# Kernel tuning notes

Hardware: AMD Instinct MI355X
Metric: run time of the kernel (lower is better)

Reference implementation:

```python
import jax, jax.numpy as jnp
import numpy as np

B, S, HID = 1, 2048, 2048
H, KH, D = 16, 8, 128          # query heads, kv heads, head_dim
GROUPS = H // KH                # num_key_value_groups = 2
EPS = 1e-6
SCALE = D ** -0.5
NEG = -1e9


def rmsnorm(x, w):
    # torch.nn.RMSNorm over last dim with learned weight
    return x * jax.lax.rsqrt(jnp.mean(x * x, axis=-1, keepdims=True) + EPS) * w


def rope(x, cos, sin):
    # x: [b, s, h, d]; cos/sin: [s, d//2]  (rotate-half style, matching apply_rotary_emb_single)
    half = x.shape[-1] // 2
    xr, xi = x[..., :half], x[..., half:]
    c = cos[None, :, None, :]
    s = sin[None, :, None, :]
    return jnp.concatenate([xr * c - xi * s, xr * s + xi * c], axis=-1)


def setup_inputs() -> dict:
    key = jax.random.key(0)
    ks = jax.random.split(key, 8)
    hidden_states = jax.random.normal(ks[0], (B, S, HID), jnp.float32)
    # real RoPE angle tables (theta=1e6, Qwen3-style), shape [S, D//2]
    inv_freq = 1.0 / (1e6 ** (np.arange(0, D, 2, dtype=np.float32) / D))
    ang = np.arange(S, dtype=np.float32)[:, None] * inv_freq[None, :]
    freqs_cos = jnp.asarray(np.cos(ang), jnp.float32)
    freqs_sin = jnp.asarray(np.sin(ang), jnp.float32)
    # additive causal mask [1, S, S]
    causal = jnp.tril(jnp.ones((S, S), jnp.bool_))
    atten_mask = jnp.where(causal, 0.0, NEG).astype(jnp.float32)[None]
    # learned params (no bias: attention_bias=False)
    Wq = jax.random.normal(ks[1], (H * D, HID), jnp.float32) * 0.02
    Wk = jax.random.normal(ks[2], (KH * D, HID), jnp.float32) * 0.02
    Wv = jax.random.normal(ks[3], (KH * D, HID), jnp.float32) * 0.02
    Wo = jax.random.normal(ks[4], (HID, H * D), jnp.float32) * 0.02
    q_norm_w = 1.0 + 0.01 * jax.random.normal(ks[5], (D,), jnp.float32)
    k_norm_w = 1.0 + 0.01 * jax.random.normal(ks[6], (D,), jnp.float32)
    return {"hidden_states": hidden_states, "freqs_cos": freqs_cos, "freqs_sin": freqs_sin,
            "atten_mask": atten_mask, "Wq": Wq, "Wk": Wk, "Wv": Wv, "Wo": Wo,
            "q_norm_w": q_norm_w, "k_norm_w": k_norm_w}


def reference(hidden_states, freqs_cos, freqs_sin, atten_mask, Wq, Wk, Wv, Wo, q_norm_w, k_norm_w):
    b, s, _ = hidden_states.shape
    q = (hidden_states @ Wq.T).reshape(b, s, H, D)
    k = (hidden_states @ Wk.T).reshape(b, s, KH, D)
    v = (hidden_states @ Wv.T).reshape(b, s, KH, D)
    q = rope(rmsnorm(q, q_norm_w), freqs_cos, freqs_sin)
    k = rope(rmsnorm(k, k_norm_w), freqs_cos, freqs_sin)
    # GQA: head i uses kv head i // GROUPS -> repeat kv heads in-order
    k_exp = jnp.repeat(k, GROUPS, axis=2)  # [b, s, H, d]
    v_exp = jnp.repeat(v, GROUPS, axis=2)
    scores = jnp.einsum('bshd,bthd->bhst', q, k_exp) * SCALE + atten_mask[:, None, :, :]
    attn = jax.nn.softmax(scores, axis=-1)
    y = jnp.einsum('bhst,bthd->bshd', attn, v_exp).reshape(b, s, H * D)
    y = y @ Wo.T
    # output_new_cache_only: last-position k (post-norm/RoPE) and raw v per kv head
    k_new = jnp.transpose(k[:, -1], (1, 0, 2))  # [KH, b, D]
    v_new = jnp.transpose(v[:, -1], (1, 0, 2))  # [KH, b, D]
    return y, k_new, v_new
```

## Files before the change

### kernel.cpp

```cpp
#include <hip/hip_runtime.h>
#include <hip/hip_bf16.h>
#include <math.h>

#define S_LEN 2048
#define HID 2048
#define NH 16
#define NKH 8
#define HD 128
#define QKV_N 4096
#define SCALE 0.08838834764831845f
#define EPS 1e-6f
#define LOG2E 1.4426950408889634f

typedef __hip_bfloat16 bf16;
typedef unsigned int u32;
typedef __bf16 bf16x8 __attribute__((ext_vector_type(8)));
typedef float f32x4 __attribute__((ext_vector_type(4)));

#define MFMA(a, b, c) __builtin_amdgcn_mfma_f32_16x16x32_bf16(a, b, c, 0, 0, 0)

static __device__ __forceinline__ bf16x8 ld_frag(const bf16* p) {
    return __builtin_bit_cast(bf16x8, *(const uint4*)p);
}

static __device__ __forceinline__ void gload_lds16(const void* g, void* l) {
    __builtin_amdgcn_global_load_lds(
        (const __attribute__((address_space(1))) u32*)g,
        (__attribute__((address_space(3))) u32*)l, 16, 0, 0);
}

__global__ __launch_bounds__(256) void cvt4(
    const float* __restrict__ s0, const float* __restrict__ s1,
    const float* __restrict__ s2, const float* __restrict__ s3,
    bf16* __restrict__ d0, bf16* __restrict__ d1,
    bf16* __restrict__ d2, bf16* __restrict__ d3)
{
    int i = blockIdx.x * 256 + threadIdx.x;
    const float* s; bf16* d; int off;
    if (i < (1 << 20))                   { s = s0; d = d0; off = 0; }
    else if (i < (2 << 20))              { s = s1; d = d1; off = 1 << 20; }
    else if (i < (2 << 20) + (1 << 19))  { s = s2; d = d2; off = 2 << 20; }
    else                                 { s = s3; d = d3; off = (2 << 20) + (1 << 19); }
    int j = i - off;
    float4 v = ((const float4*)s)[j];
    bf16* p = d + 4 * (size_t)j;
    p[0] = __float2bfloat16(v.x);
    p[1] = __float2bfloat16(v.y);
    p[2] = __float2bfloat16(v.z);
    p[3] = __float2bfloat16(v.w);
}

__global__ __launch_bounds__(256) void cvt_bf16(
    const float* __restrict__ src, bf16* __restrict__ dst, int n4)
{
    int i = blockIdx.x * 256 + threadIdx.x;
    if (i < n4) {
        float4 v = ((const float4*)src)[i];
        bf16* d = dst + 4 * (size_t)i;
        d[0] = __float2bfloat16(v.x);
        d[1] = __float2bfloat16(v.y);
        d[2] = __float2bfloat16(v.z);
        d[3] = __float2bfloat16(v.w);
    }
}

template <int BF16OUT>
__global__ __launch_bounds__(256) void gemm_m97(
    const bf16* __restrict__ A, const bf16* __restrict__ B,
    void* __restrict__ Cv, int M, int N, int K)
{
    __shared__ bf16 As[128 * 32];
    __shared__ bf16 Bs[128 * 32];
    const int tid = threadIdx.x;
    const int n0 = blockIdx.x * 128, m0 = blockIdx.y * 128;
    const int w = tid >> 6, lane = tid & 63;
    const int l15 = lane & 15, quad = lane >> 4;
    const int wr = (w >> 1) * 64, wc = (w & 1) * 64;

    f32x4 acc[4][4];
    #pragma unroll
    for (int i = 0; i < 4; ++i)
        #pragma unroll
        for (int j = 0; j < 4; ++j)
            acc[i][j] = f32x4{0.f, 0.f, 0.f, 0.f};

    const int grow = lane >> 2;
    const int gcol = ((lane & 3) ^ ((lane >> 3) & 3)) * 8;
    const int fcol = (quad ^ ((l15 >> 1) & 3)) * 8;

    for (int k0 = 0; k0 < K; k0 += 32) {
        __syncthreads();
        #pragma unroll
        for (int j = 0; j < 2; ++j) {
            int c = 2 * w + j;
            int row = 16 * c + grow;
            gload_lds16(A + (size_t)(m0 + row) * K + k0 + gcol, &As[c * 512]);
            gload_lds16(B + (size_t)(n0 + row) * K + k0 + gcol, &Bs[c * 512]);
        }
        __syncthreads();

        bf16x8 av[4], bv[4];
        #pragma unroll
        for (int i = 0; i < 4; ++i)
            av[i] = ld_frag(&As[(wr + i * 16 + l15) * 32 + fcol]);
        #pragma unroll
        for (int j = 0; j < 4; ++j)
            bv[j] = ld_frag(&Bs[(wc + j * 16 + l15) * 32 + fcol]);
        #pragma unroll
        for (int i = 0; i < 4; ++i)
            #pragma unroll
            for (int j = 0; j < 4; ++j)
                acc[i][j] = MFMA(av[i], bv[j], acc[i][j]);
    }

    #pragma unroll
    for (int i = 0; i < 4; ++i)
        #pragma unroll
        for (int j = 0; j < 4; ++j)
            #pragma unroll
            for (int r = 0; r < 4; ++r) {
                int row = m0 + wr + i * 16 + quad * 4 + r;
                int col = n0 + wc + j * 16 + l15;
                if (BF16OUT)
                    ((bf16*)Cv)[(size_t)row * N + col] = __float2bfloat16(acc[i][j][r]);
                else
                    ((float*)Cv)[(size_t)row * N + col] = acc[i][j][r];
            }
}

__global__ __launch_bounds__(256, 3) void gemm_n64(
    const bf16* __restrict__ A, const bf16* __restrict__ B,
    float* __restrict__ C, int M, int N, int K)
{
    __shared__ bf16 As[128 * 32];
    __shared__ bf16 Bs[64 * 32];
    const int tid = threadIdx.x;
    const int n0 = blockIdx.x * 64, m0 = blockIdx.y * 128;
    const int w = tid >> 6, lane = tid & 63;
    const int l15 = lane & 15, quad = lane >> 4;

    f32x4 acc[2][4];
    #pragma unroll
    for (int i = 0; i < 2; ++i)
        #pragma unroll
        for (int j = 0; j < 4; ++j)
            acc[i][j] = f32x4{0.f, 0.f, 0.f, 0.f};

    const int grow = lane >> 2;
    const int gcol = ((lane & 3) ^ ((lane >> 3) & 3)) * 8;
    const int fcol = (quad ^ ((l15 >> 1) & 3)) * 8;

    for (int k0 = 0; k0 < K; k0 += 32) {
        __syncthreads();
        #pragma unroll
        for (int j = 0; j < 3; ++j) {
            int c = 3 * w + j;
            if (c < 8) {
                int row = 16 * c + grow;
                gload_lds16(A + (size_t)(m0 + row) * K + k0 + gcol, &As[c * 512]);
            } else {
                int row = 16 * (c - 8) + grow;
                gload_lds16(B + (size_t)(n0 + row) * K + k0 + gcol, &Bs[(c - 8) * 512]);
            }
        }
        __syncthreads();

        bf16x8 av[2], bv[4];
        #pragma unroll
        for (int i = 0; i < 2; ++i)
            av[i] = ld_frag(&As[(w * 32 + i * 16 + l15) * 32 + fcol]);
        #pragma unroll
        for (int j = 0; j < 4; ++j)
            bv[j] = ld_frag(&Bs[(j * 16 + l15) * 32 + fcol]);
        #pragma unroll
        for (int i = 0; i < 2; ++i)
            #pragma unroll
            for (int j = 0; j < 4; ++j)
                acc[i][j] = MFMA(av[i], bv[j], acc[i][j]);
    }

    #pragma unroll
    for (int i = 0; i < 2; ++i)
        #pragma unroll
        for (int j = 0; j < 4; ++j)
            #pragma unroll
            for (int r = 0; r < 4; ++r)
                C[(size_t)(m0 + w * 32 + i * 16 + quad * 4 + r) * N +
                  n0 + j * 16 + l15] = acc[i][j][r];
}

__global__ __launch_bounds__(128) void norm_rope(
    bf16* __restrict__ qkvb,
    const float* __restrict__ cosb, const float* __restrict__ sinb,
    const float* __restrict__ qw, const float* __restrict__ kw,
    float* __restrict__ knew, float* __restrict__ vnew)
{
    const int s = blockIdx.x;
    const int h = blockIdx.y;
    const int d = threadIdx.x;

    bf16* row;
    const float* wgt;
    int kh = -1;
    if (h < NH) {
        row = qkvb + (size_t)s * QKV_N + h * HD;
        wgt = qw;
    } else {
        kh = h - NH;
        row = qkvb + (size_t)s * QKV_N + HID + kh * HD;
        wgt = kw;
    }

    float x = __bfloat162float(row[d]);
    float ss = x * x;
    #pragma unroll
    for (int off = 32; off >= 1; off >>= 1) ss += __shfl_xor(ss, off, 64);

    __shared__ float sred[2];
    __shared__ float xn[128];
    int lane = d & 63, wid = d >> 6;
    if (lane == 0) sred[wid] = ss;
    __syncthreads();
    float total = sred[0] + sred[1];
    float rr = rsqrtf(total * (1.0f / 128.0f) + EPS);
    xn[d] = x * rr * wgt[d];
    __syncthreads();

    float res;
    if (d < 64) {
        float c = cosb[s * 64 + d], sn = sinb[s * 64 + d];
        res = xn[d] * c - xn[d + 64] * sn;
    } else {
        int d2 = d - 64;
        float c = cosb[s * 64 + d2], sn = sinb[s * 64 + d2];
        res = xn[d2] * sn + xn[d] * c;
    }

    float store_val = (h < NH) ? res * SCALE : res;
    row[d] = __float2bfloat16(store_val);

    if (kh >= 0 && s == S_LEN - 1) {
        knew[kh * HD + d] = res;
        vnew[kh * HD + d] =
            __bfloat162float(qkvb[(size_t)s * QKV_N + HID + NKH * HD + kh * HD + d]);
    }
}

__global__ __launch_bounds__(256) void transpose_v(
    const bf16* __restrict__ qkvb, bf16* __restrict__ vT)
{
    const int r0 = blockIdx.x * 64;
    const int s0 = blockIdx.y * 32;
    const int rl = threadIdx.x & 63, sg = threadIdx.x >> 6;

    union { uint4 u; bf16 b[8]; } pk;
    #pragma unroll
    for (int j = 0; j < 8; ++j)
        pk.b[j] = qkvb[(size_t)(s0 + sg * 8 + j) * QKV_N + HID + NKH * HD + r0 + rl];
    *(uint4*)(vT + (size_t)(r0 + rl) * S_LEN + s0 + sg * 8) = pk.u;
}

__global__ __launch_bounds__(256, 2) void attn_mfma(
    const bf16* __restrict__ qkvb, const bf16* __restrict__ vT,
    bf16* __restrict__ outb)
{
    __shared__ bf16 Ks[2][64 * 128];
    __shared__ bf16 Vs[2][128 * 64];
    __shared__ bf16 Ps[4][16 * 72];

    const int x = blockIdx.x;
    const int h = blockIdx.y, kvh = h >> 1;
    int a = (x & 1) ? (31 - (x >> 1)) : (x >> 1);
    const int qb = (h < 8) ? a : 31 - a;
    const int tid = threadIdx.x, w = tid >> 6, lane = tid & 63;
    const int l15 = lane & 15, quad = lane >> 4;
    const int qw0 = qb * 64 + w * 16;

    bf16x8 qf[4];
    #pragma unroll
    for (int dk = 0; dk < 4; ++dk)
        qf[dk] = ld_frag(qkvb + (size_t)(qw0 + l15) * QKV_N +
                         h * HD + dk * 32 + quad * 8);

    f32x4 o[8];
    #pragma unroll
    for (int dt = 0; dt < 8; ++dt) o[dt] = f32x4{0.f, 0.f, 0.f, 0.f};
    float m_st = -1e30f, l_st = 0.f;

    auto stage = [&](int t, int nb) {
        const int kt0 = t * 64;
        if (w < 2) {
            #pragma unroll
            for (int c = 0; c < 8; ++c) {
                int chunk = w * 8 + c;
                int row = 4 * chunk + (lane >> 4);
                int ls = (lane & 15) ^ (row & 15);
                gload_lds16(qkvb + (size_t)(kt0 + row) * QKV_N + HID +
                            kvh * HD + ls * 8,
                            &Ks[nb][chunk * 512]);
            }
        } else {
            #pragma unroll
            for (int c = 0; c < 8; ++c) {
                int chunk = (w - 2) * 8 + c;
                int row = 8 * chunk + (lane >> 3);
                int ls = (lane & 7) ^ ((lane >> 3) & 7);
                gload_lds16(vT + (size_t)(kvh * HD + row) * S_LEN + kt0 + ls * 8,
                            &Vs[nb][chunk * 512]);
            }
        }
    };

    stage(0, 0);

    for (int t = 0; t <= qb; ++t) {
        const int pp = t & 1;
        __syncthreads();
        if (t < qb) stage(t + 1, pp ^ 1);

        f32x4 sc[4];
        #pragma unroll
        for (int mt = 0; mt < 4; ++mt) sc[mt] = f32x4{0.f, 0.f, 0.f, 0.f};
        #pragma unroll
        for (int dk = 0; dk < 4; ++dk)
            #pragma unroll
            for (int mt = 0; mt < 4; ++mt) {
                bf16x8 kf = ld_frag(&Ks[pp][(mt * 16 + l15) * 128 +
                                            (((dk * 4 + quad) ^ l15) * 8)]);
                sc[mt] = MFMA(kf, qf[dk], sc[mt]);
            }

        if (t == qb) {
            #pragma unroll
            for (int mt = 0; mt < 4; ++mt)
                #pragma unroll
                for (int r = 0; r < 4; ++r) {
                    int kg = t * 64 + mt * 16 + quad * 4 + r;
                    if (kg > qw0 + l15) sc[mt][r] = -1e30f;
                }
        }

        float mx = -1e30f;
        #pragma unroll
        for (int mt = 0; mt < 4; ++mt)
            #pragma unroll
            for (int r = 0; r < 4; ++r) mx = fmaxf(mx, sc[mt][r]);
        mx = fmaxf(mx, __shfl_xor(mx, 16, 64));
        mx = fmaxf(mx, __shfl_xor(mx, 32, 64));
        float mnew = fmaxf(m_st, mx);
        float al = exp2f((m_st - mnew) * LOG2E);
        m_st = mnew;
        float rs = 0.f;
        #pragma unroll
        for (int mt = 0; mt < 4; ++mt) {
            union { uint2 u; bf16 hh[4]; } pk;
            #pragma unroll
            for (int r = 0; r < 4; ++r) {
                float p = exp2f((sc[mt][r] - mnew) * LOG2E);
                pk.hh[r] = __float2bfloat16(p);
                rs += p;
            }
            *(uint2*)&Ps[w][l15 * 72 + mt * 16 + quad * 4] = pk.u;
        }
        rs += __shfl_xor(rs, 16, 64);
        rs += __shfl_xor(rs, 32, 64);
        l_st = l_st * al + rs;

        #pragma unroll
        for (int dt = 0; dt < 8; ++dt)
            #pragma unroll
            for (int r = 0; r < 4; ++r) o[dt][r] *= al;

        #pragma unroll
        for (int kc = 0; kc < 2; ++kc) {
            bf16x8 pf = ld_frag(&Ps[w][l15 * 72 + kc * 32 + quad * 8]);
            #pragma unroll
            for (int dt = 0; dt < 8; ++dt) {
                bf16x8 vf = ld_frag(&Vs[pp][(dt * 16 + l15) * 64 +
                                            (((kc * 4 + quad) ^ (l15 & 7)) * 8)]);
                o[dt] = MFMA(vf, pf, o[dt]);
            }
        }
    }

    float inv = 1.0f / l_st;
    int qg = qw0 + l15;
    #pragma unroll
    for (int dt = 0; dt < 8; ++dt) {
        union { uint2 u; bf16 hh[4]; } pk;
        #pragma unroll
        for (int r = 0; r < 4; ++r)
            pk.hh[r] = __float2bfloat16(o[dt][r] * inv);
        *(uint2*)&outb[(size_t)qg * HID + h * HD + dt * 16 + quad * 4] = pk.u;
    }
}

extern "C" void kernel_launch(void* const* d_in, const int* in_sizes, int n_in,
                              void* d_out, int out_size, void* d_ws, size_t ws_size,
                              hipStream_t stream) {
    const float* hidden = (const float*)d_in[0];
    const float* fcos   = (const float*)d_in[1];
    const float* fsin   = (const float*)d_in[2];
    const float* Wq = (const float*)d_in[4];
    const float* Wk = (const float*)d_in[5];
    const float* Wv = (const float*)d_in[6];
    const float* Wo = (const float*)d_in[7];
    const float* qw = (const float*)d_in[8];
    const float* kw = (const float*)d_in[9];
    float* out = (float*)d_out;

    bf16* qkvb  = (bf16*)d_ws;
    bf16* vT    = qkvb + (size_t)S_LEN * QKV_N;
    bf16* attnb = vT + (size_t)NKH * HD * S_LEN;
    bf16* wqkvb = attnb + (size_t)S_LEN * HID;
    bf16* hidb  = wqkvb + (size_t)QKV_N * HID;

    float* knew = out + (size_t)S_LEN * HID;
    float* vnew = knew + NKH * HD;

    cvt4<<<12288, 256, 0, stream>>>(
        hidden, Wq, Wk, Wv,
        hidb, wqkvb, wqkvb + (size_t)HID * HID,
        wqkvb + (size_t)(HID + NKH * HD) * HID);

    gemm_m97<1><<<dim3(QKV_N / 128, S_LEN / 128), 256, 0, stream>>>(
        hidb, wqkvb, qkvb, S_LEN, QKV_N, HID);

    cvt_bf16<<<(HID * HID / 4) / 256, 256, 0, stream>>>(Wo, hidb, HID * HID / 4);

    norm_rope<<<dim3(S_LEN, NH + NKH), 128, 0, stream>>>(
        qkvb, fcos, fsin, qw, kw, knew, vnew);

    transpose_v<<<dim3((NKH * HD) / 64, S_LEN / 32), 256, 0, stream>>>(qkvb, vT);

    attn_mfma<<<dim3(32, NH), 256, 0, stream>>>(qkvb, vT, attnb);

    gemm_n64<<<dim3(HID / 64, S_LEN / 128), 256, 0, stream>>>(
        attnb, hidb, out, S_LEN, HID, HID);
}
```

Measured before the change: 293.6 us.

## Fuse norm, RoPE and V transpose into QKV GEMM epilogue; shrink attention KV tile

The QKV GEMM now gives each warp full 128-column head rows, so RMSNorm, RoPE and scaling run in its epilogue. V tiles are written transposed directly, which removes the norm_rope and transpose_v kernels. The Wo conversion is folded into the single conversion kernel, using a separate buffer. Attention switches to 32-key tiles with smaller LDS, occupancy 3, and per-warp skipping of fully masked tiles. The GEMM warp layout changes from 2x2 to 4x1, which needs more B-fragment LDS reads, and the attention loop now runs twice as many iterations, each with a sync.

```diff
diff --git a/kernel.cpp b/kernel.cpp
--- a/kernel.cpp
+++ b/kernel.cpp
@@ -29,18 +29,20 @@
         (__attribute__((address_space(3))) u32*)l, 16, 0, 0);
 }
 
-__global__ __launch_bounds__(256) void cvt4(
+__global__ __launch_bounds__(256) void cvt5(
     const float* __restrict__ s0, const float* __restrict__ s1,
     const float* __restrict__ s2, const float* __restrict__ s3,
-    bf16* __restrict__ d0, bf16* __restrict__ d1,
-    bf16* __restrict__ d2, bf16* __restrict__ d3)
+    const float* __restrict__ s4,
+    bf16* __restrict__ d0, bf16* __restrict__ d1, bf16* __restrict__ d2,
+    bf16* __restrict__ d3, bf16* __restrict__ d4)
 {
     int i = blockIdx.x * 256 + threadIdx.x;
     const float* s; bf16* d; int off;
     if (i < (1 << 20))                   { s = s0; d = d0; off = 0; }
     else if (i < (2 << 20))              { s = s1; d = d1; off = 1 << 20; }
     else if (i < (2 << 20) + (1 << 19))  { s = s2; d = d2; off = 2 << 20; }
-    else                                 { s = s3; d = d3; off = (2 << 20) + (1 << 19); }
+    else if (i < (3 << 20))              { s = s3; d = d3; off = (2 << 20) + (1 << 19); }
+    else                                 { s = s4; d = d4; off = 3 << 20; }
     int j = i - off;
     float4 v = ((const float4*)s)[j];
     bf16* p = d + 4 * (size_t)j;
@@ -50,24 +52,12 @@
     p[3] = __float2bfloat16(v.w);
 }
 
-__global__ __launch_bounds__(256) void cvt_bf16(
-    const float* __restrict__ src, bf16* __restrict__ dst, int n4)
-{
-    int i = blockIdx.x * 256 + threadIdx.x;
-    if (i < n4) {
-        float4 v = ((const float4*)src)[i];
-        bf16* d = dst + 4 * (size_t)i;
-        d[0] = __float2bfloat16(v.x);
-        d[1] = __float2bfloat16(v.y);
-        d[2] = __float2bfloat16(v.z);
-        d[3] = __float2bfloat16(v.w);
-    }
-}
-
-template <int BF16OUT>
-__global__ __launch_bounds__(256) void gemm_m97(
+__global__ __launch_bounds__(256) void gemm_qkv(
     const bf16* __restrict__ A, const bf16* __restrict__ B,
-    void* __restrict__ Cv, int M, int N, int K)
+    bf16* __restrict__ qkvb, bf16* __restrict__ vT,
+    const float* __restrict__ fcos, const float* __restrict__ fsin,
+    const float* __restrict__ qw, const float* __restrict__ kw,
+    float* __restrict__ knew, float* __restrict__ vnew)
 {
     __shared__ bf16 As[128 * 32];
     __shared__ bf16 Bs[128 * 32];
@@ -75,57 +65,108 @@
     const int n0 = blockIdx.x * 128, m0 = blockIdx.y * 128;
     const int w = tid >> 6, lane = tid & 63;
     const int l15 = lane & 15, quad = lane >> 4;
-    const int wr = (w >> 1) * 64, wc = (w & 1) * 64;
-
-    f32x4 acc[4][4];
-    #pragma unroll
-    for (int i = 0; i < 4; ++i)
-        #pragma unroll
-        for (int j = 0; j < 4; ++j)
+
+    f32x4 acc[2][8];
+    #pragma unroll
+    for (int i = 0; i < 2; ++i)
+        #pragma unroll
+        for (int j = 0; j < 8; ++j)
             acc[i][j] = f32x4{0.f, 0.f, 0.f, 0.f};
 
     const int grow = lane >> 2;
     const int gcol = ((lane & 3) ^ ((lane >> 3) & 3)) * 8;
     const int fcol = (quad ^ ((l15 >> 1) & 3)) * 8;
 
-    for (int k0 = 0; k0 < K; k0 += 32) {
+    for (int k0 = 0; k0 < HID; k0 += 32) {
         __syncthreads();
         #pragma unroll
         for (int j = 0; j < 2; ++j) {
             int c = 2 * w + j;
             int row = 16 * c + grow;
-            gload_lds16(A + (size_t)(m0 + row) * K + k0 + gcol, &As[c * 512]);
-            gload_lds16(B + (size_t)(n0 + row) * K + k0 + gcol, &Bs[c * 512]);
+            gload_lds16(A + (size_t)(m0 + row) * HID + k0 + gcol, &As[c * 512]);
+            gload_lds16(B + (size_t)(n0 + row) * HID + k0 + gcol, &Bs[c * 512]);
         }
         __syncthreads();
 
-        bf16x8 av[4], bv[4];
-        #pragma unroll
-        for (int i = 0; i < 4; ++i)
-            av[i] = ld_frag(&As[(wr + i * 16 + l15) * 32 + fcol]);
-        #pragma unroll
-        for (int j = 0; j < 4; ++j)
-            bv[j] = ld_frag(&Bs[(wc + j * 16 + l15) * 32 + fcol]);
-        #pragma unroll
-        for (int i = 0; i < 4; ++i)
-            #pragma unroll
-            for (int j = 0; j < 4; ++j)
+        bf16x8 av[2], bv[8];
+        #pragma unroll
+        for (int i = 0; i < 2; ++i)
+            av[i] = ld_frag(&As[(w * 32 + i * 16 + l15) * 32 + fcol]);
+        #pragma unroll
+        for (int j = 0; j < 8; ++j)
+            bv[j] = ld_frag(&Bs[(j * 16 + l15) * 32 + fcol]);
+        #pragma unroll
+        for (int i = 0; i < 2; ++i)
+            #pragma unroll
+            for (int j = 0; j < 8; ++j)
                 acc[i][j] = MFMA(av[i], bv[j], acc[i][j]);
     }
 
-    #pragma unroll
-    for (int i = 0; i < 4; ++i)
-        #pragma unroll
-        for (int j = 0; j < 4; ++j)
+    const int hblk = n0 >> 7;
+    if (hblk < 24) {
+        const float* wgt = (hblk < 16) ? qw : kw;
+        float wv[8];
+        #pragma unroll
+        for (int j = 0; j < 8; ++j) wv[j] = wgt[j * 16 + l15];
+        const size_t cb = (hblk < 16) ? (size_t)hblk * HD
+                                      : (size_t)HID + (size_t)(hblk - 16) * HD;
+        #pragma unroll
+        for (int i = 0; i < 2; ++i)
             #pragma unroll
             for (int r = 0; r < 4; ++r) {
-                int row = m0 + wr + i * 16 + quad * 4 + r;
-                int col = n0 + wc + j * 16 + l15;
-                if (BF16OUT)
-                    ((bf16*)Cv)[(size_t)row * N + col] = __float2bfloat16(acc[i][j][r]);
-                else
-                    ((float*)Cv)[(size_t)row * N + col] = acc[i][j][r];
-            }
+                int srow = m0 + w * 32 + i * 16 + quad * 4 + r;
+                float ss = 0.f;
+                #pragma unroll
+                for (int j = 0; j < 8; ++j) ss += acc[i][j][r] * acc[i][j][r];
+                ss += __shfl_xor(ss, 1);
+                ss += __shfl_xor(ss, 2);
+                ss += __shfl_xor(ss, 4);
+                ss += __shfl_xor(ss, 8);
+                float rr = rsqrtf(ss * (1.0f / 128.0f) + EPS);
+                float x[8], res[8];
+                #pragma unroll
+                for (int j = 0; j < 8; ++j) x[j] = acc[i][j][r] * rr * wv[j];
+                #pragma unroll
+                for (int jj = 0; jj < 4; ++jj) {
+                    float c = fcos[srow * 64 + jj * 16 + l15];
+                    float s = fsin[srow * 64 + jj * 16 + l15];
+                    res[jj]     = x[jj] * c - x[jj + 4] * s;
+                    res[jj + 4] = x[jj] * s + x[jj + 4] * c;
+                }
+                if (hblk < 16) {
+                    #pragma unroll
+                    for (int j = 0; j < 8; ++j)
+                        qkvb[(size_t)srow * QKV_N + cb + j * 16 + l15] =
+                            __float2bfloat16(res[j] * SCALE);
+                } else {
+                    #pragma unroll
+                    for (int j = 0; j < 8; ++j)
+                        qkvb[(size_t)srow * QKV_N + cb + j * 16 + l15] =
+                            __float2bfloat16(res[j]);
+                    if (srow == S_LEN - 1) {
+                        #pragma unroll
+                        for (int j = 0; j < 8; ++j)
+                            knew[(hblk - 16) * HD + j * 16 + l15] = res[j];
+                    }
+                }
+            }
+    } else {
+        const int kh = hblk - 24;
+        #pragma unroll
+        for (int i = 0; i < 2; ++i)
+            #pragma unroll
+            for (int j = 0; j < 8; ++j) {
+                int d = j * 16 + l15;
+                int rowbase = m0 + w * 32 + i * 16 + quad * 4;
+                union { uint2 u; bf16 hh[4]; } pk;
+                #pragma unroll
+                for (int r = 0; r < 4; ++r)
+                    pk.hh[r] = __float2bfloat16(acc[i][j][r]);
+                *(uint2*)&vT[(size_t)(kh * HD + d) * S_LEN + rowbase] = pk.u;
+                if (rowbase == S_LEN - 4)
+                    vnew[kh * HD + d] = acc[i][j][3];
+            }
+    }
 }
 
 __global__ __launch_bounds__(256, 3) void gemm_n64(
@@ -189,84 +230,13 @@
                   n0 + j * 16 + l15] = acc[i][j][r];
 }
 
-__global__ __launch_bounds__(128) void norm_rope(
-    bf16* __restrict__ qkvb,
-    const float* __restrict__ cosb, const float* __restrict__ sinb,
-    const float* __restrict__ qw, const float* __restrict__ kw,
-    float* __restrict__ knew, float* __restrict__ vnew)
-{
-    const int s = blockIdx.x;
-    const int h = blockIdx.y;
-    const int d = threadIdx.x;
-
-    bf16* row;
-    const float* wgt;
-    int kh = -1;
-    if (h < NH) {
-        row = qkvb + (size_t)s * QKV_N + h * HD;
-        wgt = qw;
-    } else {
-        kh = h - NH;
-        row = qkvb + (size_t)s * QKV_N + HID + kh * HD;
-        wgt = kw;
-    }
-
-    float x = __bfloat162float(row[d]);
-    float ss = x * x;
-    #pragma unroll
-    for (int off = 32; off >= 1; off >>= 1) ss += __shfl_xor(ss, off, 64);
-
-    __shared__ float sred[2];
-    __shared__ float xn[128];
-    int lane = d & 63, wid = d >> 6;
-    if (lane == 0) sred[wid] = ss;
-    __syncthreads();
-    float total = sred[0] + sred[1];
-    float rr = rsqrtf(total * (1.0f / 128.0f) + EPS);
-    xn[d] = x * rr * wgt[d];
-    __syncthreads();
-
-    float res;
-    if (d < 64) {
-        float c = cosb[s * 64 + d], sn = sinb[s * 64 + d];
-        res = xn[d] * c - xn[d + 64] * sn;
-    } else {
-        int d2 = d - 64;
-        float c = cosb[s * 64 + d2], sn = sinb[s * 64 + d2];
-        res = xn[d2] * sn + xn[d] * c;
-    }
-
-    float store_val = (h < NH) ? res * SCALE : res;
-    row[d] = __float2bfloat16(store_val);
-
-    if (kh >= 0 && s == S_LEN - 1) {
-        knew[kh * HD + d] = res;
-        vnew[kh * HD + d] =
-            __bfloat162float(qkvb[(size_t)s * QKV_N + HID + NKH * HD + kh * HD + d]);
-    }
-}
-
-__global__ __launch_bounds__(256) void transpose_v(
-    const bf16* __restrict__ qkvb, bf16* __restrict__ vT)
-{
-    const int r0 = blockIdx.x * 64;
-    const int s0 = blockIdx.y * 32;
-    const int rl = threadIdx.x & 63, sg = threadIdx.x >> 6;
-
-    union { uint4 u; bf16 b[8]; } pk;
-    #pragma unroll
-    for (int j = 0; j < 8; ++j)
-        pk.b[j] = qkvb[(size_t)(s0 + sg * 8 + j) * QKV_N + HID + NKH * HD + r0 + rl];
-    *(uint4*)(vT + (size_t)(r0 + rl) * S_LEN + s0 + sg * 8) = pk.u;
-}
-
-__global__ __launch_bounds__(256, 2) void attn_mfma(
+__global__ __launch_bounds__(256, 3) void attn_mfma(
     const bf16* __restrict__ qkvb, const bf16* __restrict__ vT,
     bf16* __restrict__ outb)
 {
-    __shared__ bf16 Ks[2][64 * 128];
-    __shared__ bf16 Vs[2][128 * 64];
-    __shared__ bf16 Ps[4][16 * 72];
+    __shared__ bf16 Ks[2][32 * 128];
+    __shared__ bf16 Vs[2][128 * 32];
+    __shared__ bf16 Ps[4][16 * 40];
 
     const int x = blockIdx.x;
     const int h = blockIdx.y, kvh = h >> 1;
@@ -288,11 +258,11 @@
     float m_st = -1e30f, l_st = 0.f;
 
     auto stage = [&](int t, int nb) {
-        const int kt0 = t * 64;
+        const int kt0 = t * 32;
         if (w < 2) {
             #pragma unroll
-            for (int c = 0; c < 8; ++c) {
-                int chunk = w * 8 + c;
+            for (int c = 0; c < 4; ++c) {
+                int chunk = w * 4 + c;
                 int row = 4 * chunk + (lane >> 4);
                 int ls = (lane & 15) ^ (row & 15);
                 gload_lds16(qkvb + (size_t)(kt0 + row) * QKV_N + HID +
@@ -301,10 +271,10 @@
             }
         } else {
             #pragma unroll
-            for (int c = 0; c < 8; ++c) {
-                int chunk = (w - 2) * 8 + c;
-                int row = 8 * chunk + (lane >> 3);
-                int ls = (lane & 7) ^ ((lane >> 3) & 7);
+            for (int c = 0; c < 4; ++c) {
+                int chunk = (w - 2) * 4 + c;
+                int row = 16 * chunk + (lane >> 2);
+                int ls = (lane & 3) ^ ((lane >> 3) & 3);
                 gload_lds16(vT + (size_t)(kvh * HD + row) * S_LEN + kt0 + ls * 8,
                             &Vs[nb][chunk * 512]);
             }
@@ -312,37 +282,39 @@
     };
 
     stage(0, 0);
-
-    for (int t = 0; t <= qb; ++t) {
+    const int tmax = 2 * qb + 1;
+    for (int t = 0; t <= tmax; ++t) {
         const int pp = t & 1;
+        const int kt0 = t * 32;
         __syncthreads();
-        if (t < qb) stage(t + 1, pp ^ 1);
-
-        f32x4 sc[4];
-        #pragma unroll
-        for (int mt = 0; mt < 4; ++mt) sc[mt] = f32x4{0.f, 0.f, 0.f, 0.f};
+        if (t < tmax) stage(t + 1, pp ^ 1);
+        if (kt0 > qw0 + 15) continue;
+
+        f32x4 sc[2];
+        sc[0] = f32x4{0.f, 0.f, 0.f, 0.f};
+        sc[1] = f32x4{0.f, 0.f, 0.f, 0.f};
         #pragma unroll
         for (int dk = 0; dk < 4; ++dk)
             #pragma unroll
-            for (int mt = 0; mt < 4; ++mt) {
+            for (int mt = 0; mt < 2; ++mt) {
                 bf16x8 kf = ld_frag(&Ks[pp][(mt * 16 + l15) * 128 +
-                                            (((dk * 4 + quad) ^ l15) * 8)]);
+                                            (((dk * 4 + quad) ^ l15) & 15) * 8]);
                 sc[mt] = MFMA(kf, qf[dk], sc[mt]);
             }
 
-        if (t == qb) {
-            #pragma unroll
-            for (int mt = 0; mt < 4; ++mt)
+        if (kt0 + 31 > qw0) {
+            #pragma unroll
+            for (int mt = 0; mt < 2; ++mt)
                 #pragma unroll
                 for (int r = 0; r < 4; ++r) {
-                    int kg = t * 64 + mt * 16 + quad * 4 + r;
+                    int kg = kt0 + mt * 16 + quad * 4 + r;
                     if (kg > qw0 + l15) sc[mt][r] = -1e30f;
                 }
         }
 
         float mx = -1e30f;
         #pragma unroll
-        for (int mt = 0; mt < 4; ++mt)
+        for (int mt = 0; mt < 2; ++mt)
             #pragma unroll
             for (int r = 0; r < 4; ++r) mx = fmaxf(mx, sc[mt][r]);
         mx = fmaxf(mx, __shfl_xor(mx, 16, 64));
@@ -352,7 +324,7 @@
         m_st = mnew;
         float rs = 0.f;
         #pragma unroll
-        for (int mt = 0; mt < 4; ++mt) {
+        for (int mt = 0; mt < 2; ++mt) {
             union { uint2 u; bf16 hh[4]; } pk;
             #pragma unroll
             for (int r = 0; r < 4; ++r) {
@@ -360,7 +332,7 @@
                 pk.hh[r] = __float2bfloat16(p);
                 rs += p;
             }
-            *(uint2*)&Ps[w][l15 * 72 + mt * 16 + quad * 4] = pk.u;
+            *(uint2*)&Ps[w][l15 * 40 + mt * 16 + quad * 4] = pk.u;
         }
         rs += __shfl_xor(rs, 16, 64);
         rs += __shfl_xor(rs, 32, 64);
@@ -371,15 +343,12 @@
             #pragma unroll
             for (int r = 0; r < 4; ++r) o[dt][r] *= al;
 
-        #pragma unroll
-        for (int kc = 0; kc < 2; ++kc) {
-            bf16x8 pf = ld_frag(&Ps[w][l15 * 72 + kc * 32 + quad * 8]);
-            #pragma unroll
-            for (int dt = 0; dt < 8; ++dt) {
-                bf16x8 vf = ld_frag(&Vs[pp][(dt * 16 + l15) * 64 +
-                                            (((kc * 4 + quad) ^ (l15 & 7)) * 8)]);
-                o[dt] = MFMA(vf, pf, o[dt]);
-            }
+        bf16x8 pf = ld_frag(&Ps[w][l15 * 40 + quad * 8]);
+        #pragma unroll
+        for (int dt = 0; dt < 8; ++dt) {
+            bf16x8 vf = ld_frag(&Vs[pp][(dt * 16 + l15) * 32 +
+                                        ((quad ^ ((l15 >> 1) & 3)) * 8)]);
+            o[dt] = MFMA(vf, pf, o[dt]);
         }
     }
 
@@ -414,27 +383,21 @@
     bf16* attnb = vT + (size_t)NKH * HD * S_LEN;
     bf16* wqkvb = attnb + (size_t)S_LEN * HID;
     bf16* hidb  = wqkvb + (size_t)QKV_N * HID;
+    bf16* wob   = hidb + (size_t)S_LEN * HID;
 
     float* knew = out + (size_t)S_LEN * HID;
     float* vnew = knew + NKH * HD;
 
-    cvt4<<<12288, 256, 0, stream>>>(
-        hidden, Wq, Wk, Wv,
+    cvt5<<<16384, 256, 0, stream>>>(
+        hidden, Wq, Wk, Wv, Wo,
         hidb, wqkvb, wqkvb + (size_t)HID * HID,
-        wqkvb + (size_t)(HID + NKH * HD) * HID);
-
-    gemm_m97<1><<<dim3(QKV_N / 128, S_LEN / 128), 256, 0, stream>>>(
-        hidb, wqkvb, qkvb, S_LEN, QKV_N, HID);
-
-    cvt_bf16<<<(HID * HID / 4) / 256, 256, 0, stream>>>(Wo, hidb, HID * HID / 4);
-
-    norm_rope<<<dim3(S_LEN, NH + NKH), 128, 0, stream>>>(
-        qkvb, fcos, fsin, qw, kw, knew, vnew);
-
-    transpose_v<<<dim3((NKH * HD) / 64, S_LEN / 32), 256, 0, stream>>>(qkvb, vT);
+        wqkvb + (size_t)(HID + NKH * HD) * HID, wob);
+
+    gemm_qkv<<<dim3(QKV_N / 128, S_LEN / 128), 256, 0, stream>>>(
+        hidb, wqkvb, qkvb, vT, fcos, fsin, qw, kw, knew, vnew);
 
     attn_mfma<<<dim3(32, NH), 256, 0, stream>>>(qkvb, vT, attnb);
 
     gemm_n64<<<dim3(HID / 64, S_LEN / 128), 256, 0, stream>>>(
-        attnb, hidb, out, S_LEN, HID, HID);
-}
+        attnb, wob, out, S_LEN, HID, HID);
+}
```

Measured after the change: 273.0 us. 7.0% less time.
